# Kernel tuning notes

Hardware: AMD Instinct MI355X
Metric: run time of the kernel (lower is better)

## Reference

```python
import jax, jax.numpy as jnp
import numpy as np

EMB_DIMS = 1024

def setup_inputs() -> dict:
    key = jax.random.key(0)
    k1, k2, k3 = jax.random.split(key, 3)
    B, S, D = 4, 2048, EMB_DIMS
    x = jax.random.normal(k1, (B, S, D), dtype=jnp.float32)
    # nn.Linear(D, 3D): weight stored as [3D, D] in torch; we use [D, 3D] (x @ W)
    w_qkv = jax.random.normal(k2, (D, 3 * D), dtype=jnp.float32) * (D ** -0.5)
    b_qkv = jax.random.normal(k3, (3 * D,), dtype=jnp.float32) * 0.01
    return {"x": x, "w_qkv": w_qkv, "b_qkv": b_qkv}

def reference(x, w_qkv, b_qkv):
    D = x.shape[-1]
    scale = D ** (-0.5)  # torch code divides qk by this (i.e. multiplies by sqrt(D))
    qkv = x @ w_qkv + b_qkv                      # [B,S,3D]
    q, k, v = jnp.split(qkv, 3, axis=-1)         # each [B,S,D]
    scores = jnp.einsum('bsd,btd->bst', q, k) / scale  # [B,S,S]
    attn = jax.nn.sigmoid(scores)                # sigmoid, NOT softmax
    return jnp.einsum('bst,btd->bsd', attn, v)   # [B,S,D]
```

## Files before the change

kernel.cpp:

```cpp
#include <hip/hip_runtime.h>
#include <stdint.h>

typedef unsigned short u16;
typedef _Float16 f16x8 __attribute__((ext_vector_type(8)));
typedef float f32x4 __attribute__((ext_vector_type(4)));

#define B_   4
#define S_   2048
#define D_   1024
#define ND3  3072

__device__ __forceinline__ u16 f2h(float x) {
    union { _Float16 h; u16 u; } v; v.h = (_Float16)x; return v.u;
}

__device__ __forceinline__ void gload_lds16(const u16* g, u16* l) {
    __builtin_amdgcn_global_load_lds((const __attribute__((address_space(1))) void*)g,
                                     (__attribute__((address_space(3))) void*)l, 16, 0, 0);
}

__device__ __forceinline__ int xcd_swz(int lid, int nwg) {
    int c = nwg >> 3;
    return (lid & 7) * c + (lid >> 3);
}

template<int NT>
__device__ __forceinline__ void gemm_wide(const u16* __restrict__ A, const u16* __restrict__ Bt,
                                          int lda, int ldb, int rowbase, int colbase,
                                          u16* ldsA, u16* ldsB, f32x4 (&acc)[4][4])
{
    const int NSTEP = 2 * NT;
    const int tid  = threadIdx.x;
    const int lane = tid & 63;
    const int w    = tid >> 6;
    const int wr   = w >> 2, wc = w & 3;

    const int r0 = tid >> 2;
    const int c0 = (((tid & 3) ^ ((tid >> 3) & 3)) << 3);
    const uint32_t offA0 = (uint32_t)(rowbase + r0) * lda + c0;
    const uint32_t offB0 = (uint32_t)(colbase + r0) * ldb + c0;
    const uint32_t offB1 = offB0 + (uint32_t)128 * ldb;
    const int dst = tid << 3;

    const int rd_lane = ((lane & 15) << 5) + ((((lane >> 4) ^ (lane >> 1)) & 3) << 3);
    const int wrOff = wr << 11;
    const int wcOff = wc << 11;

#define ISSUE(sv) do { int s_ = (sv); \
    if (s_ < NSTEP) { \
        uint32_t ko_ = (uint32_t)s_ << 5; \
        int slA_ = (s_ & 1) << 12, slB_ = (s_ & 1) << 13; \
        gload_lds16(A  + offA0 + ko_, ldsA + slA_ + dst); \
        gload_lds16(Bt + offB0 + ko_, ldsB + slB_ + dst); \
        gload_lds16(Bt + offB1 + ko_, ldsB + slB_ + dst + 4096); \
    } } while (0)

    f16x8 af[4], bf[4];

#define STEP(sv, slA, slB) { \
    asm volatile("s_waitcnt lgkmcnt(0)" ::: "memory"); \
    __builtin_amdgcn_s_barrier(); \
    asm volatile("" ::: "memory"); \
    ISSUE((sv) + 1); \
    if ((sv) < NSTEP - 1) asm volatile("s_waitcnt vmcnt(3)" ::: "memory"); \
    else                  asm volatile("s_waitcnt vmcnt(0)" ::: "memory"); \
    __builtin_amdgcn_s_barrier(); \
    asm volatile("" ::: "memory"); \
    _Pragma("unroll") for (int mq = 0; mq < 4; ++mq) \
        af[mq] = *(const f16x8*)(ldsA + (slA) + wrOff + (mq << 9) + rd_lane); \
    _Pragma("unroll") for (int n = 0; n < 4; ++n) \
        bf[n] = *(const f16x8*)(ldsB + (slB) + wcOff + (n << 9) + rd_lane); \
    _Pragma("unroll") for (int mq = 0; mq < 4; ++mq) \
    _Pragma("unroll") for (int n = 0; n < 4; ++n) \
        acc[mq][n] = __builtin_amdgcn_mfma_f32_16x16x32_f16(af[mq], bf[n], acc[mq][n], 0, 0, 0); }

    ISSUE(0);
    for (int T = 0; T < NT; ++T) {
        STEP(2 * T,     0,    0)
        STEP(2 * T + 1, 4096, 8192)
    }
#undef STEP
#undef ISSUE
}

template<int NT>
__device__ __forceinline__ void gemm_narrow(const u16* __restrict__ A, const u16* __restrict__ Bt,
                                            int lda, int ldb, int rowbase, int colbase,
                                            u16* ldsA, u16* ldsB, f32x4 (&acc)[4][2])
{
    const int NSTEP = 2 * NT;
    const int tid  = threadIdx.x;
    const int lane = tid & 63;
    const int w    = tid >> 6;
    const int wr   = w >> 2, wc = w & 3;

    const int r0 = tid >> 2;
    const int c0 = (((tid & 3) ^ ((tid >> 3) & 3)) << 3);
    const uint32_t offA0 = (uint32_t)(rowbase + r0) * lda + c0;
    const uint32_t offB0 = (uint32_t)(colbase + r0) * ldb + c0;
    const int dst = tid << 3;

    const int rd_lane = ((lane & 15) << 5) + ((((lane >> 4) ^ (lane >> 1)) & 3) << 3);
    const int wrOff = wr << 11;
    const int wcOff = wc << 10;

#define ISSUE(sv) do { int s_ = (sv); \
    if (s_ < NSTEP) { \
        uint32_t ko_ = (uint32_t)s_ << 5; \
        int sl_ = (s_ & 1) << 12; \
        gload_lds16(A  + offA0 + ko_, ldsA + sl_ + dst); \
        gload_lds16(Bt + offB0 + ko_, ldsB + sl_ + dst); \
    } } while (0)

    f16x8 af[4], bf[2];

#define STEP(sv, sl) { \
    asm volatile("s_waitcnt lgkmcnt(0)" ::: "memory"); \
    __builtin_amdgcn_s_barrier(); \
    asm volatile("" ::: "memory"); \
    ISSUE((sv) + 1); \
    if ((sv) < NSTEP - 1) asm volatile("s_waitcnt vmcnt(2)" ::: "memory"); \
    else                  asm volatile("s_waitcnt vmcnt(0)" ::: "memory"); \
    __builtin_amdgcn_s_barrier(); \
    asm volatile("" ::: "memory"); \
    _Pragma("unroll") for (int mq = 0; mq < 4; ++mq) \
        af[mq] = *(const f16x8*)(ldsA + (sl) + wrOff + (mq << 9) + rd_lane); \
    _Pragma("unroll") for (int n = 0; n < 2; ++n) \
        bf[n] = *(const f16x8*)(ldsB + (sl) + wcOff + (n << 9) + rd_lane); \
    _Pragma("unroll") for (int mq = 0; mq < 4; ++mq) \
    _Pragma("unroll") for (int n = 0; n < 2; ++n) \
        acc[mq][n] = __builtin_amdgcn_mfma_f32_16x16x32_f16(af[mq], bf[n], acc[mq][n], 0, 0, 0); }

    ISSUE(0);
    for (int T = 0; T < NT; ++T) {
        STEP(2 * T,     0)
        STEP(2 * T + 1, 4096)
    }
#undef STEP
#undef ISSUE
}

__global__ __launch_bounds__(256) void k_cvt_f16(const float* __restrict__ in,
                                                 u16* __restrict__ oh, int n) {
    int i = (blockIdx.x * 256 + threadIdx.x) << 3;
    if (i >= n) return;
    float4 a = *(const float4*)(in + i);
    float4 b = *(const float4*)(in + i + 4);
    ushort4 h0, h1;
    h0.x = f2h(a.x); h0.y = f2h(a.y); h0.z = f2h(a.z); h0.w = f2h(a.w);
    h1.x = f2h(b.x); h1.y = f2h(b.y); h1.z = f2h(b.z); h1.w = f2h(b.w);
    *(ushort4*)(oh + i)     = h0;
    *(ushort4*)(oh + i + 4) = h1;
}

__global__ __launch_bounds__(256) void k_transpose_f16(const float* __restrict__ W,
                                                       u16* __restrict__ Wt, int R, int C) {
    __shared__ float t[32][33];
    int tx = threadIdx.x & 31, ty = threadIdx.x >> 5;
    int c0 = blockIdx.x << 5, r0 = blockIdx.y << 5;
#pragma unroll
    for (int i = 0; i < 4; ++i) {
        int r = (i << 3) + ty;
        t[r][tx] = W[(size_t)(r0 + r) * C + c0 + tx];
    }
    __syncthreads();
#pragma unroll
    for (int i = 0; i < 4; ++i) {
        int r = (i << 3) + ty;
        Wt[(size_t)(c0 + r) * R + r0 + tx] = f2h(t[tx][r]);
    }
}

__global__ __launch_bounds__(512, 4) void k_qkv(const u16* __restrict__ xh,
                                                const u16* __restrict__ wt,
                                                const float* __restrict__ bias,
                                                u16* __restrict__ qf, u16* __restrict__ kf,
                                                u16* __restrict__ vt) {
    __shared__ u16 lds[24576];
    f32x4 acc[4][4];
    f32x4 z = {0.f, 0.f, 0.f, 0.f};
#pragma unroll
    for (int m = 0; m < 4; ++m)
#pragma unroll
        for (int n = 0; n < 4; ++n) acc[m][n] = z;

    const int lid = blockIdx.y * 12 + blockIdx.x;
    const int swz = xcd_swz(lid, 768);
    const int bx = swz % 12, by = swz / 12;
    const int rowbase = by << 7;
    const int colbase = bx << 8;
    gemm_wide<16>(xh, wt, D_, D_, rowbase, colbase, lds, lds + 8192, acc);

    const int lane = threadIdx.x & 63;
    const int w = threadIdx.x >> 6;
    const int wr = w >> 2, wc = w & 3;
    const int region = colbase >> 10;
#pragma unroll
    for (int m = 0; m < 4; ++m) {
        int gr0 = rowbase + wr * 64 + m * 16 + ((lane >> 4) << 2);
#pragma unroll
        for (int n = 0; n < 4; ++n) {
            int gc = colbase + wc * 64 + n * 16 + (lane & 15);
            float bv = bias[gc];
            if (region == 0) {
#pragma unroll
                for (int r = 0; r < 4; ++r)
                    qf[(size_t)(gr0 + r) * D_ + gc] = f2h(acc[m][n][r] + bv);
            } else if (region == 1) {
                int c = gc - 1024;
#pragma unroll
                for (int r = 0; r < 4; ++r)
                    kf[(size_t)(gr0 + r) * D_ + c] = f2h(acc[m][n][r] + bv);
            } else {
                int d  = gc - 2048;
                int b  = gr0 >> 11;
                int t0 = gr0 & 2047;
                size_t base = (((size_t)b << 10) + d) * (size_t)S_ + t0;
#pragma unroll
                for (int r = 0; r < 4; ++r)
                    vt[base + r] = f2h(acc[m][n][r] + bv);
            }
        }
    }
}

__global__ __launch_bounds__(512, 4) void k_scores(const u16* __restrict__ qf,
                                                   const u16* __restrict__ kf,
                                                   u16* __restrict__ attn) {
    __shared__ u16 lds[24576];
    f32x4 acc[4][4];
    f32x4 z = {0.f, 0.f, 0.f, 0.f};
#pragma unroll
    for (int m = 0; m < 4; ++m)
#pragma unroll
        for (int n = 0; n < 4; ++n) acc[m][n] = z;

    const int m_ = (blockIdx.z << 4) + blockIdx.y;
    const int P  = (blockIdx.x << 3) + (m_ >> 3);
    const int bx = m_ & 7, by = P & 15, b = P >> 4;

    const size_t boff = (size_t)b * S_ * D_;
    u16* att = attn + (size_t)b * S_ * S_;
    const int rowbase = by << 7, colbase = bx << 8;
    gemm_wide<16>(qf + boff, kf + boff, D_, D_, rowbase, colbase, lds, lds + 8192, acc);

    const int lane = threadIdx.x & 63;
    const int w = threadIdx.x >> 6;
    const int wr = w >> 2, wc = w & 3;
#pragma unroll
    for (int m = 0; m < 4; ++m) {
        int gr0 = rowbase + wr * 64 + m * 16 + ((lane >> 4) << 2);
#pragma unroll
        for (int n = 0; n < 4; ++n) {
            int gc = colbase + wc * 64 + n * 16 + (lane & 15);
#pragma unroll
            for (int r = 0; r < 4; ++r) {
                float sv = acc[m][n][r] * 32.0f;
                float sg = 1.0f / (1.0f + __expf(-sv));
                att[(size_t)(gr0 + r) * S_ + gc] = f2h(sg);
            }
        }
    }
}

__global__ __launch_bounds__(512, 4) void k_pv(const u16* __restrict__ attn,
                                               const u16* __restrict__ vt,
                                               float* __restrict__ out) {
    __shared__ u16 lds[16384];
    f32x4 acc[4][2];
    f32x4 z = {0.f, 0.f, 0.f, 0.f};
#pragma unroll
    for (int m = 0; m < 4; ++m)
#pragma unroll
        for (int n = 0; n < 2; ++n) acc[m][n] = z;

    const int m_ = (blockIdx.z << 4) + blockIdx.y;
    const int P  = (blockIdx.x << 3) + (m_ >> 3);
    const int bx = m_ & 7, by = P & 15, b = P >> 4;

    const u16* Aa = attn + (size_t)b * S_ * S_;
    const u16* Bv = vt   + (size_t)b * D_ * S_;
    float* ob     = out  + (size_t)b * S_ * D_;
    const int rowbase = by << 7, colbase = bx << 7;
    gemm_narrow<32>(Aa, Bv, S_, S_, rowbase, colbase, lds, lds + 8192, acc);

    const int lane = threadIdx.x & 63;
    const int w = threadIdx.x >> 6;
    const int wr = w >> 2, wc = w & 3;
#pragma unroll
    for (int m = 0; m < 4; ++m) {
        int gr0 = rowbase + wr * 64 + m * 16 + ((lane >> 4) << 2);
#pragma unroll
        for (int n = 0; n < 2; ++n) {
            int gc = colbase + wc * 32 + n * 16 + (lane & 15);
#pragma unroll
            for (int r = 0; r < 4; ++r)
                ob[(size_t)(gr0 + r) * D_ + gc] = acc[m][n][r];
        }
    }
}

extern "C" void kernel_launch(void* const* d_in, const int* in_sizes, int n_in,
                              void* d_out, int out_size, void* d_ws, size_t ws_size,
                              hipStream_t stream) {
    const float* x    = (const float*)d_in[0];
    const float* wqkv = (const float*)d_in[1];
    const float* bias = (const float*)d_in[2];
    float* out = (float*)d_out;

    const size_t MB = 1048576;
    uint8_t* ws = (uint8_t*)d_ws;
    u16* xh   = (u16*)(ws);
    u16* wt   = (u16*)(ws + 16 * MB);
    u16* qf   = (u16*)(ws + 32 * MB);
    u16* kf   = (u16*)(ws + 48 * MB);
    u16* vt   = (u16*)(ws + 64 * MB);
    u16* attn = (u16*)(ws);

    k_cvt_f16<<<dim3(4096), dim3(256), 0, stream>>>(x, xh, B_ * S_ * D_);
    k_transpose_f16<<<dim3(ND3 / 32, D_ / 32), dim3(256), 0, stream>>>(wqkv, wt, D_, ND3);
    k_qkv<<<dim3(ND3 / 256, (B_ * S_) / 128), dim3(512), 0, stream>>>(xh, wt, bias, qf, kf, vt);
    k_scores<<<dim3(S_ / 256, S_ / 128, B_), dim3(512), 0, stream>>>(qf, kf, attn);
    k_pv<<<dim3(D_ / 128, S_ / 128, B_), dim3(512), 0, stream>>>(attn, vt, out);
}
```

Before: 161.1 us.

## Switch GEMM main loops to triple-buffered LDS with one barrier per step

```diff
diff --git a/kernel.cpp b/kernel.cpp
--- a/kernel.cpp
+++ b/kernel.cpp
@@ -49,7 +49,9 @@
 #define ISSUE(sv) do { int s_ = (sv); \
     if (s_ < NSTEP) { \
         uint32_t ko_ = (uint32_t)s_ << 5; \
-        int slA_ = (s_ & 1) << 12, slB_ = (s_ & 1) << 13; \
+        int st_ = s_ % 3; \
+        int slA_ = st_ << 12;              \
+        int slB_ = st_ << 13;              \
         gload_lds16(A  + offA0 + ko_, ldsA + slA_ + dst); \
         gload_lds16(Bt + offB0 + ko_, ldsB + slB_ + dst); \
         gload_lds16(Bt + offB1 + ko_, ldsB + slB_ + dst + 4096); \
@@ -57,29 +59,29 @@
 
     f16x8 af[4], bf[4];
 
-#define STEP(sv, slA, slB) { \
-    asm volatile("s_waitcnt lgkmcnt(0)" ::: "memory"); \
-    __builtin_amdgcn_s_barrier(); \
-    asm volatile("" ::: "memory"); \
-    ISSUE((sv) + 1); \
-    if ((sv) < NSTEP - 1) asm volatile("s_waitcnt vmcnt(3)" ::: "memory"); \
-    else                  asm volatile("s_waitcnt vmcnt(0)" ::: "memory"); \
-    __builtin_amdgcn_s_barrier(); \
-    asm volatile("" ::: "memory"); \
-    _Pragma("unroll") for (int mq = 0; mq < 4; ++mq) \
-        af[mq] = *(const f16x8*)(ldsA + (slA) + wrOff + (mq << 9) + rd_lane); \
-    _Pragma("unroll") for (int n = 0; n < 4; ++n) \
-        bf[n] = *(const f16x8*)(ldsB + (slB) + wcOff + (n << 9) + rd_lane); \
-    _Pragma("unroll") for (int mq = 0; mq < 4; ++mq) \
-    _Pragma("unroll") for (int n = 0; n < 4; ++n) \
-        acc[mq][n] = __builtin_amdgcn_mfma_f32_16x16x32_f16(af[mq], bf[n], acc[mq][n], 0, 0, 0); }
-
-    ISSUE(0);
-    for (int T = 0; T < NT; ++T) {
-        STEP(2 * T,     0,    0)
-        STEP(2 * T + 1, 4096, 8192)
-    }
-#undef STEP
+    ISSUE(0); ISSUE(1);
+    int sl = 0;
+    for (int S = 0; S < NSTEP; ++S) {
+        asm volatile("s_waitcnt lgkmcnt(0)" ::: "memory");
+        if (S < NSTEP - 1) asm volatile("s_waitcnt vmcnt(3)" ::: "memory");
+        else               asm volatile("s_waitcnt vmcnt(0)" ::: "memory");
+        __builtin_amdgcn_s_barrier();
+        asm volatile("" ::: "memory");
+        ISSUE(S + 2);
+        const int slA = sl << 12, slB = sl << 13;
+#pragma unroll
+        for (int mq = 0; mq < 4; ++mq)
+            af[mq] = *(const f16x8*)(ldsA + slA + wrOff + (mq << 9) + rd_lane);
+#pragma unroll
+        for (int n = 0; n < 4; ++n)
+            bf[n] = *(const f16x8*)(ldsB + slB + wcOff + (n << 9) + rd_lane);
+#pragma unroll
+        for (int mq = 0; mq < 4; ++mq)
+#pragma unroll
+            for (int n = 0; n < 4; ++n)
+                acc[mq][n] = __builtin_amdgcn_mfma_f32_16x16x32_f16(af[mq], bf[n], acc[mq][n], 0, 0, 0);
+        sl = (sl == 2) ? 0 : sl + 1;
+    }
 #undef ISSUE
 }
 
@@ -107,36 +109,36 @@
 #define ISSUE(sv) do { int s_ = (sv); \
     if (s_ < NSTEP) { \
         uint32_t ko_ = (uint32_t)s_ << 5; \
-        int sl_ = (s_ & 1) << 12; \
+        int sl_ = (s_ % 3) << 12; \
         gload_lds16(A  + offA0 + ko_, ldsA + sl_ + dst); \
         gload_lds16(Bt + offB0 + ko_, ldsB + sl_ + dst); \
     } } while (0)
 
     f16x8 af[4], bf[2];
 
-#define STEP(sv, sl) { \
-    asm volatile("s_waitcnt lgkmcnt(0)" ::: "memory"); \
-    __builtin_amdgcn_s_barrier(); \
-    asm volatile("" ::: "memory"); \
-    ISSUE((sv) + 1); \
-    if ((sv) < NSTEP - 1) asm volatile("s_waitcnt vmcnt(2)" ::: "memory"); \
-    else                  asm volatile("s_waitcnt vmcnt(0)" ::: "memory"); \
-    __builtin_amdgcn_s_barrier(); \
-    asm volatile("" ::: "memory"); \
-    _Pragma("unroll") for (int mq = 0; mq < 4; ++mq) \
-        af[mq] = *(const f16x8*)(ldsA + (sl) + wrOff + (mq << 9) + rd_lane); \
-    _Pragma("unroll") for (int n = 0; n < 2; ++n) \
-        bf[n] = *(const f16x8*)(ldsB + (sl) + wcOff + (n << 9) + rd_lane); \
-    _Pragma("unroll") for (int mq = 0; mq < 4; ++mq) \
-    _Pragma("unroll") for (int n = 0; n < 2; ++n) \
-        acc[mq][n] = __builtin_amdgcn_mfma_f32_16x16x32_f16(af[mq], bf[n], acc[mq][n], 0, 0, 0); }
-
-    ISSUE(0);
-    for (int T = 0; T < NT; ++T) {
-        STEP(2 * T,     0)
-        STEP(2 * T + 1, 4096)
-    }
-#undef STEP
+    ISSUE(0); ISSUE(1);
+    int sl = 0;
+    for (int S = 0; S < NSTEP; ++S) {
+        asm volatile("s_waitcnt lgkmcnt(0)" ::: "memory");
+        if (S < NSTEP - 1) asm volatile("s_waitcnt vmcnt(2)" ::: "memory");
+        else               asm volatile("s_waitcnt vmcnt(0)" ::: "memory");
+        __builtin_amdgcn_s_barrier();
+        asm volatile("" ::: "memory");
+        ISSUE(S + 2);
+        const int slo = sl << 12;
+#pragma unroll
+        for (int mq = 0; mq < 4; ++mq)
+            af[mq] = *(const f16x8*)(ldsA + slo + wrOff + (mq << 9) + rd_lane);
+#pragma unroll
+        for (int n = 0; n < 2; ++n)
+            bf[n] = *(const f16x8*)(ldsB + slo + wcOff + (n << 9) + rd_lane);
+#pragma unroll
+        for (int mq = 0; mq < 4; ++mq)
+#pragma unroll
+            for (int n = 0; n < 2; ++n)
+                acc[mq][n] = __builtin_amdgcn_mfma_f32_16x16x32_f16(af[mq], bf[n], acc[mq][n], 0, 0, 0);
+        sl = (sl == 2) ? 0 : sl + 1;
+    }
 #undef ISSUE
 }
 
@@ -176,7 +178,7 @@
                                                 const float* __restrict__ bias,
                                                 u16* __restrict__ qf, u16* __restrict__ kf,
                                                 u16* __restrict__ vt) {
-    __shared__ u16 lds[24576];
+    __shared__ u16 lds[36864];
     f32x4 acc[4][4];
     f32x4 z = {0.f, 0.f, 0.f, 0.f};
 #pragma unroll
@@ -189,7 +191,7 @@
     const int bx = swz % 12, by = swz / 12;
     const int rowbase = by << 7;
     const int colbase = bx << 8;
-    gemm_wide<16>(xh, wt, D_, D_, rowbase, colbase, lds, lds + 8192, acc);
+    gemm_wide<16>(xh, wt, D_, D_, rowbase, colbase, lds, lds + 12288, acc);
 
     const int lane = threadIdx.x & 63;
     const int w = threadIdx.x >> 6;
@@ -227,7 +229,7 @@
 __global__ __launch_bounds__(512, 4) void k_scores(const u16* __restrict__ qf,
                                                    const u16* __restrict__ kf,
                                                    u16* __restrict__ attn) {
-    __shared__ u16 lds[24576];
+    __shared__ u16 lds[36864];
     f32x4 acc[4][4];
     f32x4 z = {0.f, 0.f, 0.f, 0.f};
 #pragma unroll
@@ -242,7 +244,7 @@
     const size_t boff = (size_t)b * S_ * D_;
     u16* att = attn + (size_t)b * S_ * S_;
     const int rowbase = by << 7, colbase = bx << 8;
-    gemm_wide<16>(qf + boff, kf + boff, D_, D_, rowbase, colbase, lds, lds + 8192, acc);
+    gemm_wide<16>(qf + boff, kf + boff, D_, D_, rowbase, colbase, lds, lds + 12288, acc);
 
     const int lane = threadIdx.x & 63;
     const int w = threadIdx.x >> 6;
@@ -266,7 +268,7 @@
 __global__ __launch_bounds__(512, 4) void k_pv(const u16* __restrict__ attn,
                                                const u16* __restrict__ vt,
                                                float* __restrict__ out) {
-    __shared__ u16 lds[16384];
+    __shared__ u16 lds[24576];
     f32x4 acc[4][2];
     f32x4 z = {0.f, 0.f, 0.f, 0.f};
 #pragma unroll
@@ -282,7 +284,7 @@
     const u16* Bv = vt   + (size_t)b * D_ * S_;
     float* ob     = out  + (size_t)b * S_ * D_;
     const int rowbase = by << 7, colbase = bx << 7;
-    gemm_narrow<32>(Aa, Bv, S_, S_, rowbase, colbase, lds, lds + 8192, acc);
+    gemm_narrow<32>(Aa, Bv, S_, S_, rowbase, colbase, lds, lds + 12288, acc);
 
     const int lane = threadIdx.x & 63;
     const int w = threadIdx.x >> 6;
```

Result: no change. 160.8 us (-0.1%).
